# Performance work log

Measured on AMD Instinct MI355X. Metric: run time of the kernel, lower is better.

The kernel has to match this reference:

```python
import jax, jax.numpy as jnp
import numpy as np

EPS = 1e-5

def gelu(x):
    return jax.nn.gelu(x, approximate=False)  # torch nn.GELU default = exact erf

def bn(x, g, b, m, v):
    # eval-mode BatchNorm1d with running stats; broadcasts over batch axis
    return (x - m) * jax.lax.rsqrt(v + EPS) * g + b

def ln(x, g, b):
    mu = jnp.mean(x, axis=-1, keepdims=True)
    var = jnp.var(x, axis=-1, keepdims=True)
    return (x - mu) * jax.lax.rsqrt(var + EPS) * g + b

def setup_inputs() -> dict:
    B, D, H, E, C = 4096, 512, 1024, 16, 20  # combined dim D = wifi(256)+rfid(256)
    key = jax.random.key(0)
    ks = iter(jax.random.split(key, 40))
    n = lambda shape, s=0.02: jax.random.normal(next(ks), shape, dtype=jnp.float32) * s
    u = lambda shape: jax.random.uniform(next(ks), shape, dtype=jnp.float32, minval=0.5, maxval=1.5)
    inp = {
        'wifi_feat': jax.random.normal(next(ks), (B, 256), dtype=jnp.float32),
        'rfid_feat': jax.random.normal(next(ks), (B, 256), dtype=jnp.float32),
        # gate: Linear(512,1024) -> LayerNorm -> GELU -> Linear(1024,16) -> Softmax
        'gate_w1': n((D, 1024)), 'gate_b1': n((1024,)),
        'gate_ln_g': 1.0 + n((1024,)), 'gate_ln_b': n((1024,)),
        'gate_w2': n((1024, E)), 'gate_b2': n((E,)),
        # experts stacked on leading E axis
        'exp_w1': n((E, D, H)), 'exp_b1': n((E, H)),
        'exp_bn1_g': 1.0 + n((E, H)), 'exp_bn1_b': n((E, H)), 'exp_bn1_m': n((E, H), 0.1), 'exp_bn1_v': u((E, H)),
        'exp_w2': n((E, H, H)), 'exp_b2': n((E, H)),
        'exp_bn2_g': 1.0 + n((E, H)), 'exp_bn2_b': n((E, H)), 'exp_bn2_m': n((E, H), 0.1), 'exp_bn2_v': u((E, H)),
        # final head: Linear(1024,512) -> BN -> GELU -> Linear(512,20)
        'fin_w1': n((H, 512)), 'fin_b1': n((512,)),
        'fin_bn_g': 1.0 + n((512,)), 'fin_bn_b': n((512,)), 'fin_bn_m': n((512,), 0.1), 'fin_bn_v': u((512,)),
        'fin_w2': n((512, C)), 'fin_b2': n((C,)),
    }
    return inp

def reference(wifi_feat, rfid_feat,
              gate_w1, gate_b1, gate_ln_g, gate_ln_b, gate_w2, gate_b2,
              exp_w1, exp_b1, exp_bn1_g, exp_bn1_b, exp_bn1_m, exp_bn1_v,
              exp_w2, exp_b2, exp_bn2_g, exp_bn2_b, exp_bn2_m, exp_bn2_v,
              fin_w1, fin_b1, fin_bn_g, fin_bn_b, fin_bn_m, fin_bn_v,
              fin_w2, fin_b2):
    TOPK = 4
    combined = jnp.concatenate([wifi_feat, rfid_feat], axis=1)  # [B, 512]
    # gate
    g = gelu(ln(combined @ gate_w1 + gate_b1, gate_ln_g, gate_ln_b))
    gate = jax.nn.softmax(g @ gate_w2 + gate_b2, axis=1)  # [B, E]
    topk_gate, topk_idx = jax.lax.top_k(gate, TOPK)  # sorted, matches torch.topk
    topk_gate = jax.nn.softmax(topk_gate, axis=1)  # [B, K]
    # dense all-expert stack (faithful to original torch.stack over experts)
    h = jnp.einsum('bi,eih->ebh', combined, exp_w1) + exp_b1[:, None, :]  # [E,B,H]
    h = gelu(bn(h, exp_bn1_g[:, None, :], exp_bn1_b[:, None, :], exp_bn1_m[:, None, :], exp_bn1_v[:, None, :]))
    h = jnp.einsum('ebh,eho->ebo', h, exp_w2) + exp_b2[:, None, :]
    h = gelu(bn(h, exp_bn2_g[:, None, :], exp_bn2_b[:, None, :], exp_bn2_m[:, None, :], exp_bn2_v[:, None, :]))
    expert_outputs = jnp.transpose(h, (1, 0, 2))  # [B, E, H]
    selected = jnp.take_along_axis(expert_outputs, topk_idx[:, :, None], axis=1)  # [B,K,H]
    fused = jnp.einsum('bkd,bk->bd', selected, topk_gate)  # [B, H]
    # final head
    o = gelu(bn(fused @ fin_w1 + fin_b1, fin_bn_g, fin_bn_b, fin_bn_m, fin_bn_v))
    return o @ fin_w2 + fin_b2  # [B, num_classes]
```

## Files before the change

kernel.cpp:

```cpp
#include <hip/hip_runtime.h>


#define EPSN 1e-5f

typedef __attribute__((ext_vector_type(8))) short v8s;
typedef __attribute__((ext_vector_type(4))) float v4f;

typedef const unsigned int __attribute__((address_space(1)))* gas_u32;
typedef unsigned int __attribute__((address_space(3)))* las_u32;

__device__ __forceinline__ void glds16(const void* g, const void* l) {
    __builtin_amdgcn_global_load_lds((gas_u32)(uintptr_t)g, (las_u32)(uintptr_t)l, 16, 0, 0);
}

__device__ __forceinline__ float gelu_f(float x) {
    return 0.5f * x * (1.0f + erff(x * 0.70710678118654752440f));
}
__device__ __forceinline__ unsigned short f2bf(float x) {
    unsigned int u = __float_as_uint(x);
    u += 0x7fffu + ((u >> 16) & 1u);
    return (unsigned short)(u >> 16);
}
__device__ __forceinline__ float bf2f(unsigned short u) {
    return __uint_as_float(((unsigned int)u) << 16);
}

__global__ __launch_bounds__(256) void concat_kernel(const float4* __restrict__ wifi,
                                                     const float4* __restrict__ rfid,
                                                     float4* __restrict__ comb,
                                                     ushort4* __restrict__ cbf,
                                                     ushort4* __restrict__ cbf3) {
    int gid = blockIdx.x * 256 + threadIdx.x;
    int b = gid >> 7, c = gid & 127;
    float4 v = (c < 64) ? wifi[b * 64 + c] : rfid[b * 64 + (c - 64)];
    comb[gid] = v;
    ushort4 hi, lo;
    hi.x = f2bf(v.x); hi.y = f2bf(v.y); hi.z = f2bf(v.z); hi.w = f2bf(v.w);
    lo.x = f2bf(v.x - bf2f(hi.x));
    lo.y = f2bf(v.y - bf2f(hi.y));
    lo.z = f2bf(v.z - bf2f(hi.z));
    lo.w = f2bf(v.w - bf2f(hi.w));
    cbf[gid] = hi;
    const long r3 = (long)b * 384 + c;
    cbf3[r3]       = hi;
    cbf3[r3 + 128] = lo;
    cbf3[r3 + 256] = hi;
}

__global__ __launch_bounds__(256) void transpose_f2b(const float* __restrict__ in,
                                                     unsigned short* __restrict__ out,
                                                     int K, int N) {
    __shared__ float t[64][65];
    int e = blockIdx.z;
    int n0 = blockIdx.x << 6, k0 = blockIdx.y << 6;
    const float* ie = in + (long)e * K * N;
    unsigned short* oe = out + (long)e * N * K;
    int tid = threadIdx.x;
    int rr = tid >> 4, cc = (tid & 15) << 2;
#pragma unroll
    for (int p = 0; p < 4; ++p) {
        int k = (p << 4) + rr;
        float4 v = *(const float4*)(ie + (long)(k0 + k) * N + n0 + cc);
        t[k][cc + 0] = v.x; t[k][cc + 1] = v.y; t[k][cc + 2] = v.z; t[k][cc + 3] = v.w;
    }
    __syncthreads();
    int n = tid >> 2, kq = (tid & 3) << 4;
    unsigned short u[16];
#pragma unroll
    for (int j = 0; j < 16; ++j) u[j] = f2bf(t[kq + j][n]);
    uint4* dst = (uint4*)(oe + (long)(n0 + n) * K + k0 + kq);
    dst[0] = ((const uint4*)u)[0];
    dst[1] = ((const uint4*)u)[1];
}

__global__ __launch_bounds__(256) void transpose_f2b_hilo(const float* __restrict__ in,
                                                          unsigned short* __restrict__ out,
                                                          int K, int N) {
    __shared__ float t[64][65];
    int n0 = blockIdx.x << 6, k0 = blockIdx.y << 6;
    int tid = threadIdx.x;
    int rr = tid >> 4, cc = (tid & 15) << 2;
#pragma unroll
    for (int p = 0; p < 4; ++p) {
        int k = (p << 4) + rr;
        float4 v = *(const float4*)(in + (long)(k0 + k) * N + n0 + cc);
        t[k][cc + 0] = v.x; t[k][cc + 1] = v.y; t[k][cc + 2] = v.z; t[k][cc + 3] = v.w;
    }
    __syncthreads();
    int n = tid >> 2, kq = (tid & 3) << 4;
    unsigned short uh[16], ul[16];
#pragma unroll
    for (int j = 0; j < 16; ++j) {
        float x = t[kq + j][n];
        unsigned short h = f2bf(x);
        uh[j] = h;
        ul[j] = f2bf(x - bf2f(h));
    }
    unsigned short* dh = out + (long)(n0 + n) * (3 * K) + k0 + kq;
    ((uint4*)dh)[0]           = ((const uint4*)uh)[0];
    ((uint4*)dh)[1]           = ((const uint4*)uh)[1];
    ((uint4*)(dh + K))[0]     = ((const uint4*)uh)[0];
    ((uint4*)(dh + K))[1]     = ((const uint4*)uh)[1];
    ((uint4*)(dh + 2 * K))[0] = ((const uint4*)ul)[0];
    ((uint4*)(dh + 2 * K))[1] = ((const uint4*)ul)[1];
}

__global__ __launch_bounds__(256) void transpose_w2g(const float* __restrict__ in,
                                                     float* __restrict__ out) {
    int gid = blockIdx.x * 256 + threadIdx.x;
    int c = gid >> 4, e = gid & 15;
    out[e * 1024 + c] = in[gid];
}

__global__ __launch_bounds__(256) void ln_topk_wave(
    const float* __restrict__ g,
    const float* __restrict__ lng, const float* __restrict__ lnb,
    const float* __restrict__ w2t, const float* __restrict__ b2,
    float* __restrict__ wout, unsigned int* __restrict__ topk)
{
    const int tid = threadIdx.x;
    const int lane = tid & 63;
    const int b = (blockIdx.x << 2) + (tid >> 6);
    const float* row = g + (long)b * 1024;
    const int c0 = lane << 2;

    float4 xv[4];
    float s = 0.f, q = 0.f;
#pragma unroll
    for (int p = 0; p < 4; ++p) {
        float4 v = *(const float4*)(row + (p << 8) + c0);
        xv[p] = v;
        s += v.x + v.y + v.z + v.w;
        q += v.x * v.x + v.y * v.y + v.z * v.z + v.w * v.w;
    }
#pragma unroll
    for (int mk = 32; mk >= 1; mk >>= 1) {
        s += __shfl_xor(s, mk);
        q += __shfl_xor(q, mk);
    }
    const float mu = s * (1.0f / 1024.0f);
    const float var = q * (1.0f / 1024.0f) - mu * mu;
    const float rstd = rsqrtf(var + EPSN);

#pragma unroll
    for (int p = 0; p < 4; ++p) {
        float4 gv = *(const float4*)(lng + (p << 8) + c0);
        float4 bv = *(const float4*)(lnb + (p << 8) + c0);
        xv[p].x = gelu_f((xv[p].x - mu) * rstd * gv.x + bv.x);
        xv[p].y = gelu_f((xv[p].y - mu) * rstd * gv.y + bv.y);
        xv[p].z = gelu_f((xv[p].z - mu) * rstd * gv.z + bv.z);
        xv[p].w = gelu_f((xv[p].w - mu) * rstd * gv.w + bv.w);
    }

    float a[16];
#pragma unroll
    for (int i = 0; i < 16; ++i) a[i] = 0.f;
#pragma unroll
    for (int p = 0; p < 4; ++p) {
        const float4 x4 = xv[p];
        const float* wp = w2t + (p << 8) + c0;
#pragma unroll
        for (int e = 0; e < 16; ++e) {
            const float4 w = *(const float4*)(wp + (e << 10));
            a[e] = fmaf(x4.x, w.x, a[e]);
            a[e] = fmaf(x4.y, w.y, a[e]);
            a[e] = fmaf(x4.z, w.z, a[e]);
            a[e] = fmaf(x4.w, w.w, a[e]);
        }
    }
#pragma unroll
    for (int mk = 32; mk >= 1; mk >>= 1) {
#pragma unroll
        for (int i = 0; i < 16; ++i) a[i] += __shfl_xor(a[i], mk);
    }
#pragma unroll
    for (int i = 0; i < 16; ++i) a[i] += b2[i];

    float m = a[0];
#pragma unroll
    for (int i = 1; i < 16; ++i) m = fmaxf(m, a[i]);
    float Z = 0.f;
#pragma unroll
    for (int i = 0; i < 16; ++i) { a[i] = expf(a[i] - m); Z += a[i]; }
    const float iZ = 1.0f / Z;
#pragma unroll
    for (int i = 0; i < 16; ++i) a[i] *= iZ;

    float tv0, tv1, tv2, tv3;
    int ti0, ti1, ti2, ti3;
#define PICK(TV, TI)                                                         \
    {   float bv = a[0]; int bi = 0;                                         \
        _Pragma("unroll")                                                    \
        for (int i = 1; i < 16; ++i) {                                       \
            bool t = a[i] > bv; bv = t ? a[i] : bv; bi = t ? i : bi;         \
        }                                                                    \
        TV = bv; TI = bi;                                                    \
        _Pragma("unroll")                                                    \
        for (int i = 0; i < 16; ++i) a[i] = (i == bi) ? -1.f : a[i];         \
    }
    PICK(tv0, ti0)
    PICK(tv1, ti1)
    PICK(tv2, ti2)
    PICK(tv3, ti3)
#undef PICK

    const float q1 = expf(tv1 - tv0);
    const float q2 = expf(tv2 - tv0);
    const float q3 = expf(tv3 - tv0);
    const float iZ2 = 1.0f / (1.0f + q1 + q2 + q3);
    if (lane < 4) {
        float wk = (lane == 0) ? 1.f : (lane == 1) ? q1 : (lane == 2) ? q2 : q3;
        wout[(b << 2) + lane] = wk * iZ2;
    }
    if (lane == 0)
        topk[b] = (unsigned)ti0 | ((unsigned)ti1 << 8) |
                  ((unsigned)ti2 << 16) | ((unsigned)ti3 << 24);
}

__global__ __launch_bounds__(256) void compact_kernel(const unsigned int* __restrict__ topk,
                                                      int* __restrict__ rows_,
                                                      int* __restrict__ counts) {
    const int e = blockIdx.x;
    const int tid = threadIdx.x;
    const int wid = tid >> 6, lane = tid & 63;
    __shared__ int wcnt[4];
    __shared__ int wbase[4];
    __shared__ int running;
    if (tid == 0) running = 0;
    __syncthreads();
    for (int c = 0; c < 16; ++c) {
        const int r = (c << 8) + tid;
        const unsigned int w = topk[r];
        int slot = -1;
        if (((w >> 0)  & 255u) == (unsigned)e) slot = (r << 2) | 0;
        if (((w >> 8)  & 255u) == (unsigned)e) slot = (r << 2) | 1;
        if (((w >> 16) & 255u) == (unsigned)e) slot = (r << 2) | 2;
        if (((w >> 24) & 255u) == (unsigned)e) slot = (r << 2) | 3;
        const unsigned long long m = __ballot(slot >= 0);
        if (lane == 0) wcnt[wid] = __popcll(m);
        __syncthreads();
        if (tid == 0) {
            int base = running;
#pragma unroll
            for (int i = 0; i < 4; ++i) { wbase[i] = base; base += wcnt[i]; }
            running = base;
        }
        __syncthreads();
        if (slot >= 0) {
            const int pref = __popcll(m & ((1ull << lane) - 1ull));
            rows_[(e << 12) + wbase[wid] + pref] = slot;
        }
        __syncthreads();
    }
    if (tid == 0) counts[e] = running;
}

#define WLG 1024
__global__ __launch_bounds__(256) void build_wl_kernel(const int* __restrict__ counts,
                                                       int* __restrict__ wl) {
    int t = threadIdx.x;
    for (int i = t; i < 8 * WLG; i += 256) wl[i] = -1;
    __syncthreads();
    if (t < 8) {
        int* wg = wl + (t << 10);
        int idx = 0;
#pragma unroll
        for (int half = 0; half < 2; ++half) {
            int e = t + (half << 3);
            int nc = (counts[e] + 63) >> 6;
            for (int mc = 0; mc < nc; ++mc)
                for (int x = 0; x < 8; ++x)
                    wg[idx++] = (e << 16) | (mc << 4) | x;
        }
    }
}

template<int ASHIFT, bool GATHER, bool OUTBF, bool WL, bool PLAIN = false>
__global__ __launch_bounds__(256) void mfma_gemm(
    const unsigned short* __restrict__ A, int K,
    const unsigned short* __restrict__ Wt, long wstride,
    const float* __restrict__ bias,
    const float* __restrict__ bng, const float* __restrict__ bnb,
    const float* __restrict__ bnm, const float* __restrict__ bnv,
    int pstride,
    void* __restrict__ outv, int ldo,
    const int* __restrict__ rows_, const int* __restrict__ counts,
    const int* __restrict__ wl, int M)
{
    constexpr int TM = 64;
    int e, m0, n0;
    if constexpr (WL) {
        int w = wl[((blockIdx.x & 7) << 10) | (blockIdx.x >> 3)];
        if (w < 0) return;
        e = w >> 16;
        m0 = ((w >> 4) & 0xfff) << 6;
        n0 = (w & 15) << 7;
    } else {
        e = blockIdx.y;
        m0 = blockIdx.x * TM;
        n0 = blockIdx.z << 7;
    }
    const int cnt = GATHER ? counts[e] : M;

    constexpr int AB_USH = 64 * 64 + 128 * 64;
    constexpr int OL_STRIDE = 136;
    constexpr int OL_USH = OUTBF ? TM * OL_STRIDE : 0;
    constexpr int SM_USH = (OL_USH > AB_USH) ? OL_USH : AB_USH;
    __shared__ __align__(16) unsigned short smem[SM_USH];
    unsigned short* Als = smem;
    unsigned short* Bls = smem + 64 * 64;
    __shared__ int rid[TM];
    __shared__ int ain[TM];

    const int tid = threadIdx.x;
    if (tid < TM) {
        int i = m0 + tid;
        int pk, ai;
        if (GATHER) {
            if (i < cnt) { pk = rows_[(e << 12) + i]; ai = pk >> ASHIFT; }
            else { pk = -1; ai = 0; }
        } else { pk = i; ai = i; }
        rid[tid] = pk;
        ain[tid] = ai;
    }
    __syncthreads();

    const int wave = tid >> 6, lane = tid & 63;
    const int wm = (wave >> 1) << 5, wn = (wave & 1) << 6;
    const int lrow = lane & 15, kch = lane >> 4;
    const int wb = wave << 9;

    const int srow = tid >> 3, spos = tid & 7;
    const int skc8 = (spos ^ (srow & 7)) << 3;

    const unsigned short* apa = A + (long)ain[srow] * K + skc8;
    const unsigned short* apb = A + (long)ain[32 + srow] * K + skc8;
    const unsigned short* Wte = Wt + (long)e * wstride;
    const unsigned short* bp0 = Wte + (long)(n0 + srow) * K + skc8;
    const unsigned short* bp1 = Wte + (long)(n0 + 32 + srow) * K + skc8;
    const unsigned short* bp2 = Wte + (long)(n0 + 64 + srow) * K + skc8;
    const unsigned short* bp3 = Wte + (long)(n0 + 96 + srow) * K + skc8;

    v4f acc[2][4] = {};

    const int nk = K >> 6;
    for (int it = 0; it < nk; ++it) {
        glds16(apa, Als + wb);
        glds16(apb, Als + 2048 + wb);
        glds16(bp0, Bls + wb);
        glds16(bp1, Bls + 2048 + wb);
        glds16(bp2, Bls + 4096 + wb);
        glds16(bp3, Bls + 6144 + wb);
        apa += 64; apb += 64; bp0 += 64; bp1 += 64; bp2 += 64; bp3 += 64;
        __syncthreads();

#pragma unroll
        for (int s = 0; s < 2; ++s) {
            const int kc = (s << 2) | kch;
            v8s av[2], bv[4];
#pragma unroll
            for (int f = 0; f < 2; ++f) {
                const int row = wm + (f << 4) + lrow;
                av[f] = *(const v8s*)(Als + row * 64 + ((kc ^ (row & 7)) << 3));
            }
#pragma unroll
            for (int f = 0; f < 4; ++f) {
                const int row = wn + (f << 4) + lrow;
                bv[f] = *(const v8s*)(Bls + row * 64 + ((kc ^ (row & 7)) << 3));
            }
#pragma unroll
            for (int fi = 0; fi < 2; ++fi)
#pragma unroll
                for (int fj = 0; fj < 4; ++fj)
                    acc[fi][fj] = __builtin_amdgcn_mfma_f32_16x16x32_bf16(
                        av[fi], bv[fj], acc[fi][fj], 0, 0, 0);
        }
        __syncthreads();
    }

    if constexpr (OUTBF) {
        unsigned short* Ols = smem;
#pragma unroll
        for (int fj = 0; fj < 4; ++fj) {
            const int c = wn + (fj << 4) + lrow;
            const int pc = e * pstride + n0 + c;
            const float bs = bias[pc];
            const float sc = bng[pc] * rsqrtf(bnv[pc] + EPSN);
            const float mn = bnm[pc], bb = bnb[pc];
#pragma unroll
            for (int fi = 0; fi < 2; ++fi) {
#pragma unroll
                for (int r = 0; r < 4; ++r) {
                    const int lr = wm + (fi << 4) + (kch << 2) + r;
                    float x = acc[fi][fj][r] + bs;
                    x = (x - mn) * sc + bb;
                    x = gelu_f(x);
                    Ols[lr * OL_STRIDE + c] = f2bf(x);
                }
            }
        }
        __syncthreads();
        const int rl = tid >> 4;
        const int c8 = (tid & 15) << 3;
#pragma unroll
        for (int p = 0; p < TM / 16; ++p) {
            const int row = (p << 4) + rl;
            const int orow = rid[row];
            if (orow >= 0) {
                uint4 v = *(const uint4*)(Ols + row * OL_STRIDE + c8);
                *(uint4*)((unsigned short*)outv + (long)orow * ldo + n0 + c8) = v;
            }
        }
    } else {
#pragma unroll
        for (int fj = 0; fj < 4; ++fj) {
            const int c = n0 + wn + (fj << 4) + lrow;
            const int pc = e * pstride + c;
            const float bs = bias[pc];
            float sc = 1.f, mn = 0.f, bb = 0.f;
            if constexpr (!PLAIN) {
                sc = bng[pc] * rsqrtf(bnv[pc] + EPSN);
                mn = bnm[pc]; bb = bnb[pc];
            }
#pragma unroll
            for (int fi = 0; fi < 2; ++fi) {
#pragma unroll
                for (int r = 0; r < 4; ++r) {
                    const int lr = wm + (fi << 4) + (kch << 2) + r;
                    const int orow = rid[lr];
                    if (orow < 0) continue;
                    float x = acc[fi][fj][r] + bs;
                    if constexpr (!PLAIN) {
                        x = (x - mn) * sc + bb;
                        x = gelu_f(x);
                    }
                    ((float*)outv)[(long)orow * ldo + c] = x;
                }
            }
        }
    }
}

__global__ __launch_bounds__(256) void combine_bf_kernel(const ushort4* __restrict__ h2b,
                                                         const float* __restrict__ w,
                                                         ushort4* __restrict__ fusedb) {
    int gid = blockIdx.x * 256 + threadIdx.x;
    int b = gid >> 8, c = gid & 255;
    float a0 = 0.f, a1 = 0.f, a2 = 0.f, a3 = 0.f;
#pragma unroll
    for (int k = 0; k < 4; ++k) {
        float wk = w[b * 4 + k];
        ushort4 v = h2b[(long)(b * 4 + k) * 256 + c];
        a0 += wk * bf2f(v.x); a1 += wk * bf2f(v.y);
        a2 += wk * bf2f(v.z); a3 += wk * bf2f(v.w);
    }
    ushort4 o;
    o.x = f2bf(a0); o.y = f2bf(a1); o.z = f2bf(a2); o.w = f2bf(a3);
    fusedb[gid] = o;
}

__global__ __launch_bounds__(256) void fin2_kernel(const float* __restrict__ o,
                                                   const float* __restrict__ w2,
                                                   const float* __restrict__ b2,
                                                   float* __restrict__ out) {
    __shared__ float ws[512 * 20];
    int tid = threadIdx.x;
    for (int i = tid; i < 512 * 20; i += 256) ws[i] = w2[i];
    __syncthreads();
    int r = blockIdx.x * 64 + (tid >> 2);
    int c0 = (tid & 3) * 5;
    float acc[5];
#pragma unroll
    for (int j = 0; j < 5; ++j) acc[j] = b2[c0 + j];
    const float* orow = o + (long)r * 512;
    for (int i = 0; i < 512; ++i) {
        float v = orow[i];
#pragma unroll
        for (int j = 0; j < 5; ++j) acc[j] += v * ws[i * 20 + c0 + j];
    }
#pragma unroll
    for (int j = 0; j < 5; ++j) out[r * 20 + c0 + j] = acc[j];
}

extern "C" void kernel_launch(void* const* d_in, const int* in_sizes, int n_in,
                              void* d_out, int out_size, void* d_ws, size_t ws_size,
                              hipStream_t stream) {
    const float* wifi    = (const float*)d_in[0];
    const float* rfid    = (const float*)d_in[1];
    const float* gate_w1 = (const float*)d_in[2];
    const float* gate_b1 = (const float*)d_in[3];
    const float* gln_g   = (const float*)d_in[4];
    const float* gln_b   = (const float*)d_in[5];
    const float* gate_w2 = (const float*)d_in[6];
    const float* gate_b2 = (const float*)d_in[7];
    const float* exp_w1  = (const float*)d_in[8];
    const float* exp_b1  = (const float*)d_in[9];
    const float* bn1g    = (const float*)d_in[10];
    const float* bn1b    = (const float*)d_in[11];
    const float* bn1m    = (const float*)d_in[12];
    const float* bn1v    = (const float*)d_in[13];
    const float* exp_w2  = (const float*)d_in[14];
    const float* exp_b2  = (const float*)d_in[15];
    const float* bn2g    = (const float*)d_in[16];
    const float* bn2b    = (const float*)d_in[17];
    const float* bn2m    = (const float*)d_in[18];
    const float* bn2v    = (const float*)d_in[19];
    const float* fin_w1  = (const float*)d_in[20];
    const float* fin_b1  = (const float*)d_in[21];
    const float* fbng    = (const float*)d_in[22];
    const float* fbnb    = (const float*)d_in[23];
    const float* fbnm    = (const float*)d_in[24];
    const float* fbnv    = (const float*)d_in[25];
    const float* fin_w2  = (const float*)d_in[26];
    const float* fin_b2  = (const float*)d_in[27];
    float* out = (float*)d_out;

    const size_t MBy = 1u << 20;
    char* W = (char*)d_ws;
    float*          combined = (float*)         (W + 0);
    unsigned short* cbf      = (unsigned short*)(W + 8 * MBy);
    unsigned short* w1t      = (unsigned short*)(W + 12 * MBy);
    unsigned short* fusedb   = (unsigned short*)(W + 12 * MBy);
    float*          obuf     = (float*)         (W + 20 * MBy);
    unsigned short* w2t      = (unsigned short*)(W + 29 * MBy);
    float*          wq       = (float*)         (W + 61 * MBy);
    int*            rows     = (int*)           (W + 61 * MBy + (1 << 16));
    int*            counts   = (int*)           (W + 61 * MBy + (1 << 16) + (1 << 18));
    int*            wl       = (int*)           (W + 61 * MBy + (1 << 16) + (1 << 18) + 256);
    unsigned int*   topk     = (unsigned int*)  (W + 61 * MBy + (6 << 16));
    float*          w2tg     = (float*)         (W + 62 * MBy);
    unsigned short* fw1t     = (unsigned short*)(W + 63 * MBy);
    unsigned short* h1bf     = (unsigned short*)(W + 65 * MBy);
    unsigned short* cbf3     = (unsigned short*)(W + 65 * MBy);
    unsigned short* w1t3     = (unsigned short*)(W + 77 * MBy);
    float*          gbuf     = (float*)         (W + 99 * MBy);
    unsigned short* h2b      = (unsigned short*)(W + 99 * MBy);

    concat_kernel<<<2048, 256, 0, stream>>>((const float4*)wifi, (const float4*)rfid,
                                            (float4*)combined, (ushort4*)cbf,
                                            (ushort4*)cbf3);

    transpose_f2b<<<dim3(16, 8, 16), 256, 0, stream>>>(exp_w1, w1t, 512, 1024);
    transpose_f2b<<<dim3(16, 16, 16), 256, 0, stream>>>(exp_w2, w2t, 1024, 1024);
    transpose_f2b<<<dim3(8, 16, 1), 256, 0, stream>>>(fin_w1, fw1t, 1024, 512);
    transpose_f2b_hilo<<<dim3(16, 8, 1), 256, 0, stream>>>(gate_w1, w1t3, 512, 1024);
    transpose_w2g<<<64, 256, 0, stream>>>(gate_w2, w2tg);

    mfma_gemm<0, false, false, false, true><<<dim3(64, 1, 8), 256, 0, stream>>>(
        cbf3, 1536, w1t3, 0, gate_b1,
        nullptr, nullptr, nullptr, nullptr, 0,
        gbuf, 1024, nullptr, nullptr, nullptr, 4096);

    ln_topk_wave<<<1024, 256, 0, stream>>>(gbuf, gln_g, gln_b, w2tg, gate_b2,
                                           wq, topk);
    compact_kernel<<<16, 256, 0, stream>>>(topk, rows, counts);
    build_wl_kernel<<<1, 256, 0, stream>>>(counts, wl);

    mfma_gemm<2, true, true, true><<<dim3(8 * WLG, 1, 1), 256, 0, stream>>>(
        cbf, 512, w1t, (long)512 * 1024, exp_b1,
        bn1g, bn1b, bn1m, bn1v, 1024,
        h1bf, 1024, rows, counts, wl, 4096);

    mfma_gemm<0, true, true, true><<<dim3(8 * WLG, 1, 1), 256, 0, stream>>>(
        h1bf, 1024, w2t, (long)1024 * 1024, exp_b2,
        bn2g, bn2b, bn2m, bn2v, 1024,
        h2b, 1024, rows, counts, wl, 4096);

    combine_bf_kernel<<<4096, 256, 0, stream>>>((const ushort4*)h2b, wq, (ushort4*)fusedb);

    mfma_gemm<0, false, false, false><<<dim3(64, 1, 4), 256, 0, stream>>>(
        fusedb, 1024, fw1t, 0, fin_b1,
        fbng, fbnb, fbnm, fbnv, 0,
        obuf, 512, nullptr, nullptr, nullptr, 4096);

    fin2_kernel<<<64, 256, 0, stream>>>(obuf, fin_w2, fin_b2, out);
}
```

Measured before the change: 445.4 us.

## Double-buffer LDS tiles in expert GEMM to overlap global loads with MFMA

```diff
diff --git a/kernel.cpp b/kernel.cpp
--- a/kernel.cpp
+++ b/kernel.cpp
@@ -302,13 +302,12 @@
     }
     const int cnt = GATHER ? counts[e] : M;
 
-    constexpr int AB_USH = 64 * 64 + 128 * 64;
+    constexpr int BUF = 64 * 64 + 128 * 64;
+    constexpr int AB_USH = 2 * BUF;
     constexpr int OL_STRIDE = 136;
     constexpr int OL_USH = OUTBF ? TM * OL_STRIDE : 0;
     constexpr int SM_USH = (OL_USH > AB_USH) ? OL_USH : AB_USH;
     __shared__ __align__(16) unsigned short smem[SM_USH];
-    unsigned short* Als = smem;
-    unsigned short* Bls = smem + 64 * 64;
     __shared__ int rid[TM];
     __shared__ int ain[TM];
 
@@ -341,19 +340,33 @@
     const unsigned short* bp2 = Wte + (long)(n0 + 64 + srow) * K + skc8;
     const unsigned short* bp3 = Wte + (long)(n0 + 96 + srow) * K + skc8;
 
+#define STAGE(d)                                                         \
+    {   unsigned short* Ad = smem + (d) * BUF;                           \
+        unsigned short* Bd = Ad + 64 * 64;                               \
+        glds16(apa, Ad + wb);                                            \
+        glds16(apb, Ad + 2048 + wb);                                     \
+        glds16(bp0, Bd + wb);                                            \
+        glds16(bp1, Bd + 2048 + wb);                                     \
+        glds16(bp2, Bd + 4096 + wb);                                     \
+        glds16(bp3, Bd + 6144 + wb);                                     \
+        apa += 64; apb += 64; bp0 += 64; bp1 += 64; bp2 += 64; bp3 += 64; }
+
     v4f acc[2][4] = {};
 
     const int nk = K >> 6;
+    STAGE(0)
     for (int it = 0; it < nk; ++it) {
-        glds16(apa, Als + wb);
-        glds16(apb, Als + 2048 + wb);
-        glds16(bp0, Bls + wb);
-        glds16(bp1, Bls + 2048 + wb);
-        glds16(bp2, Bls + 4096 + wb);
-        glds16(bp3, Bls + 6144 + wb);
-        apa += 64; apb += 64; bp0 += 64; bp1 += 64; bp2 += 64; bp3 += 64;
-        __syncthreads();
-
+        const int cur = it & 1;
+        if (it + 1 < nk) {
+            STAGE(cur ^ 1)
+            asm volatile("s_waitcnt vmcnt(6)" ::: "memory");
+        } else {
+            asm volatile("s_waitcnt vmcnt(0)" ::: "memory");
+        }
+        asm volatile("s_barrier" ::: "memory");
+
+        const unsigned short* Als = smem + cur * BUF;
+        const unsigned short* Bls = Als + 64 * 64;
 #pragma unroll
         for (int s = 0; s < 2; ++s) {
             const int kc = (s << 2) | kch;
@@ -375,8 +388,9 @@
                     acc[fi][fj] = __builtin_amdgcn_mfma_f32_16x16x32_bf16(
                         av[fi], bv[fj], acc[fi][fj], 0, 0, 0);
         }
-        __syncthreads();
-    }
+        asm volatile("s_barrier" ::: "memory");
+    }
+#undef STAGE
 
     if constexpr (OUTBF) {
         unsigned short* Ols = smem;
```

After: 438.2 us. No clear change (-1.6%).

## Enlarge GEMM M-tile to 128 rows with 4x4 MFMA fragments per wave

Applied to the files above, without the earlier changes.

```diff
diff --git a/kernel.cpp b/kernel.cpp
--- a/kernel.cpp
+++ b/kernel.cpp
@@ -267,7 +267,7 @@
 #pragma unroll
         for (int half = 0; half < 2; ++half) {
             int e = t + (half << 3);
-            int nc = (counts[e] + 63) >> 6;
+            int nc = (counts[e] + 127) >> 7;
             for (int mc = 0; mc < nc; ++mc)
                 for (int x = 0; x < 8; ++x)
                     wg[idx++] = (e << 16) | (mc << 4) | x;
@@ -287,13 +287,13 @@
     const int* __restrict__ rows_, const int* __restrict__ counts,
     const int* __restrict__ wl, int M)
 {
-    constexpr int TM = 64;
+    constexpr int TM = 128;
     int e, m0, n0;
     if constexpr (WL) {
         int w = wl[((blockIdx.x & 7) << 10) | (blockIdx.x >> 3)];
         if (w < 0) return;
         e = w >> 16;
-        m0 = ((w >> 4) & 0xfff) << 6;
+        m0 = ((w >> 4) & 0xfff) << 7;
         n0 = (w & 15) << 7;
     } else {
         e = blockIdx.y;
@@ -302,13 +302,10 @@
     }
     const int cnt = GATHER ? counts[e] : M;
 
-    constexpr int AB_USH = 64 * 64 + 128 * 64;
+    constexpr int A_USH = 128 * 64;
+    constexpr int AB_USH = 2 * A_USH;
     constexpr int OL_STRIDE = 136;
-    constexpr int OL_USH = OUTBF ? TM * OL_STRIDE : 0;
-    constexpr int SM_USH = (OL_USH > AB_USH) ? OL_USH : AB_USH;
-    __shared__ __align__(16) unsigned short smem[SM_USH];
-    unsigned short* Als = smem;
-    unsigned short* Bls = smem + 64 * 64;
+    __shared__ __align__(16) unsigned short smem[AB_USH];
     __shared__ int rid[TM];
     __shared__ int ain[TM];
 
@@ -326,50 +323,55 @@
     __syncthreads();
 
     const int wave = tid >> 6, lane = tid & 63;
-    const int wm = (wave >> 1) << 5, wn = (wave & 1) << 6;
+    const int wm = (wave >> 1) << 6, wn = (wave & 1) << 6;
     const int lrow = lane & 15, kch = lane >> 4;
     const int wb = wave << 9;
 
     const int srow = tid >> 3, spos = tid & 7;
     const int skc8 = (spos ^ (srow & 7)) << 3;
 
-    const unsigned short* apa = A + (long)ain[srow] * K + skc8;
-    const unsigned short* apb = A + (long)ain[32 + srow] * K + skc8;
+    const unsigned short* ap0 = A + (long)ain[srow] * K + skc8;
+    const unsigned short* ap1 = A + (long)ain[32 + srow] * K + skc8;
+    const unsigned short* ap2 = A + (long)ain[64 + srow] * K + skc8;
+    const unsigned short* ap3 = A + (long)ain[96 + srow] * K + skc8;
     const unsigned short* Wte = Wt + (long)e * wstride;
-    const unsigned short* bp0 = Wte + (long)(n0 + srow) * K + skc8;
-    const unsigned short* bp1 = Wte + (long)(n0 + 32 + srow) * K + skc8;
-    const unsigned short* bp2 = Wte + (long)(n0 + 64 + srow) * K + skc8;
-    const unsigned short* bp3 = Wte + (long)(n0 + 96 + srow) * K + skc8;
-
-    v4f acc[2][4] = {};
+    const unsigned short* bq0 = Wte + (long)(n0 + srow) * K + skc8;
+    const unsigned short* bq1 = Wte + (long)(n0 + 32 + srow) * K + skc8;
+    const unsigned short* bq2 = Wte + (long)(n0 + 64 + srow) * K + skc8;
+    const unsigned short* bq3 = Wte + (long)(n0 + 96 + srow) * K + skc8;
+
+    unsigned short* Als = smem;
+    unsigned short* Bls = smem + A_USH;
+
+    v4f acc[4][4] = {};
 
     const int nk = K >> 6;
     for (int it = 0; it < nk; ++it) {
-        glds16(apa, Als + wb);
-        glds16(apb, Als + 2048 + wb);
-        glds16(bp0, Bls + wb);
-        glds16(bp1, Bls + 2048 + wb);
-        glds16(bp2, Bls + 4096 + wb);
-        glds16(bp3, Bls + 6144 + wb);
-        apa += 64; apb += 64; bp0 += 64; bp1 += 64; bp2 += 64; bp3 += 64;
+        glds16(ap0, Als + wb);
+        glds16(ap1, Als + 2048 + wb);
+        glds16(ap2, Als + 4096 + wb);
+        glds16(ap3, Als + 6144 + wb);
+        glds16(bq0, Bls + wb);
+        glds16(bq1, Bls + 2048 + wb);
+        glds16(bq2, Bls + 4096 + wb);
+        glds16(bq3, Bls + 6144 + wb);
+        ap0 += 64; ap1 += 64; ap2 += 64; ap3 += 64;
+        bq0 += 64; bq1 += 64; bq2 += 64; bq3 += 64;
         __syncthreads();
 
 #pragma unroll
         for (int s = 0; s < 2; ++s) {
             const int kc = (s << 2) | kch;
-            v8s av[2], bv[4];
-#pragma unroll
-            for (int f = 0; f < 2; ++f) {
-                const int row = wm + (f << 4) + lrow;
-                av[f] = *(const v8s*)(Als + row * 64 + ((kc ^ (row & 7)) << 3));
-            }
-#pragma unroll
-            for (int f = 0; f < 4; ++f) {
-                const int row = wn + (f << 4) + lrow;
-                bv[f] = *(const v8s*)(Bls + row * 64 + ((kc ^ (row & 7)) << 3));
-            }
-#pragma unroll
-            for (int fi = 0; fi < 2; ++fi)
+            const int sw = (kc ^ (lrow & 7)) << 3;
+            v8s av[4], bv[4];
+#pragma unroll
+            for (int f = 0; f < 4; ++f)
+                av[f] = *(const v8s*)(Als + (wm + (f << 4) + lrow) * 64 + sw);
+#pragma unroll
+            for (int f = 0; f < 4; ++f)
+                bv[f] = *(const v8s*)(Bls + (wn + (f << 4) + lrow) * 64 + sw);
+#pragma unroll
+            for (int fi = 0; fi < 4; ++fi)
 #pragma unroll
                 for (int fj = 0; fj < 4; ++fj)
                     acc[fi][fj] = __builtin_amdgcn_mfma_f32_16x16x32_bf16(
@@ -381,35 +383,41 @@
     if constexpr (OUTBF) {
         unsigned short* Ols = smem;
 #pragma unroll
-        for (int fj = 0; fj < 4; ++fj) {
-            const int c = wn + (fj << 4) + lrow;
-            const int pc = e * pstride + n0 + c;
-            const float bs = bias[pc];
-            const float sc = bng[pc] * rsqrtf(bnv[pc] + EPSN);
-            const float mn = bnm[pc], bb = bnb[pc];
-#pragma unroll
-            for (int fi = 0; fi < 2; ++fi) {
-#pragma unroll
-                for (int r = 0; r < 4; ++r) {
-                    const int lr = wm + (fi << 4) + (kch << 2) + r;
-                    float x = acc[fi][fj][r] + bs;
-                    x = (x - mn) * sc + bb;
-                    x = gelu_f(x);
-                    Ols[lr * OL_STRIDE + c] = f2bf(x);
+        for (int h = 0; h < 2; ++h) {
+            if ((wave >> 1) == h) {
+#pragma unroll
+                for (int fj = 0; fj < 4; ++fj) {
+                    const int c = wn + (fj << 4) + lrow;
+                    const int pc = e * pstride + n0 + c;
+                    const float bs = bias[pc];
+                    const float sc = bng[pc] * rsqrtf(bnv[pc] + EPSN);
+                    const float mn = bnm[pc], bb = bnb[pc];
+#pragma unroll
+                    for (int fi = 0; fi < 4; ++fi) {
+#pragma unroll
+                        for (int r = 0; r < 4; ++r) {
+                            const int lrl = (fi << 4) + (kch << 2) + r;
+                            float x = acc[fi][fj][r] + bs;
+                            x = (x - mn) * sc + bb;
+                            x = gelu_f(x);
+                            Ols[lrl * OL_STRIDE + c] = f2bf(x);
+                        }
+                    }
                 }
             }
-        }
-        __syncthreads();
-        const int rl = tid >> 4;
-        const int c8 = (tid & 15) << 3;
-#pragma unroll
-        for (int p = 0; p < TM / 16; ++p) {
-            const int row = (p << 4) + rl;
-            const int orow = rid[row];
-            if (orow >= 0) {
-                uint4 v = *(const uint4*)(Ols + row * OL_STRIDE + c8);
-                *(uint4*)((unsigned short*)outv + (long)orow * ldo + n0 + c8) = v;
+            __syncthreads();
+            const int rl = tid >> 4;
+            const int c8 = (tid & 15) << 3;
+#pragma unroll
+            for (int p = 0; p < 4; ++p) {
+                const int row = (p << 4) + rl;
+                const int orow = rid[(h << 6) + row];
+                if (orow >= 0) {
+                    uint4 v = *(const uint4*)(Ols + row * OL_STRIDE + c8);
+                    *(uint4*)((unsigned short*)outv + (long)orow * ldo + n0 + c8) = v;
+                }
             }
+            __syncthreads();
         }
     } else {
 #pragma unroll
@@ -423,7 +431,7 @@
                 mn = bnm[pc]; bb = bnb[pc];
             }
 #pragma unroll
-            for (int fi = 0; fi < 2; ++fi) {
+            for (int fi = 0; fi < 4; ++fi) {
 #pragma unroll
                 for (int r = 0; r < 4; ++r) {
                     const int lr = wm + (fi << 4) + (kch << 2) + r;
@@ -546,7 +554,7 @@
     transpose_f2b_hilo<<<dim3(16, 8, 1), 256, 0, stream>>>(gate_w1, w1t3, 512, 1024);
     transpose_w2g<<<64, 256, 0, stream>>>(gate_w2, w2tg);
 
-    mfma_gemm<0, false, false, false, true><<<dim3(64, 1, 8), 256, 0, stream>>>(
+    mfma_gemm<0, false, false, false, true><<<dim3(32, 1, 8), 256, 0, stream>>>(
         cbf3, 1536, w1t3, 0, gate_b1,
         nullptr, nullptr, nullptr, nullptr, 0,
         gbuf, 1024, nullptr, nullptr, nullptr, 4096);
@@ -556,19 +564,19 @@
     compact_kernel<<<16, 256, 0, stream>>>(topk, rows, counts);
     build_wl_kernel<<<1, 256, 0, stream>>>(counts, wl);
 
-    mfma_gemm<2, true, true, true><<<dim3(8 * WLG, 1, 1), 256, 0, stream>>>(
+    mfma_gemm<2, true, true, true><<<dim3(4096, 1, 1), 256, 0, stream>>>(
         cbf, 512, w1t, (long)512 * 1024, exp_b1,
         bn1g, bn1b, bn1m, bn1v, 1024,
         h1bf, 1024, rows, counts, wl, 4096);
 
-    mfma_gemm<0, true, true, true><<<dim3(8 * WLG, 1, 1), 256, 0, stream>>>(
+    mfma_gemm<0, true, true, true><<<dim3(4096, 1, 1), 256, 0, stream>>>(
         h1bf, 1024, w2t, (long)1024 * 1024, exp_b2,
         bn2g, bn2b, bn2m, bn2v, 1024,
         h2b, 1024, rows, counts, wl, 4096);
 
     combine_bf_kernel<<<4096, 256, 0, stream>>>((const ushort4*)h2b, wq, (ushort4*)fusedb);
 
-    mfma_gemm<0, false, false, false><<<dim3(64, 1, 4), 256, 0, stream>>>(
+    mfma_gemm<0, false, false, false><<<dim3(32, 1, 4), 256, 0, stream>>>(
         fusedb, 1024, fw1t, 0, fin_b1,
         fbng, fbnb, fbnm, fbnv, 0,
         obuf, 512, nullptr, nullptr, nullptr, 4096);
```

After: 740.3 us. 66.2% more time.

## Compact expert work list, shrink GEMM grids, and streamline top-k row compaction

Applied to the files above, without the earlier changes.

```diff
diff --git a/kernel.cpp b/kernel.cpp
--- a/kernel.cpp
+++ b/kernel.cpp
@@ -27,13 +27,11 @@
 
 __global__ __launch_bounds__(256) void concat_kernel(const float4* __restrict__ wifi,
                                                      const float4* __restrict__ rfid,
-                                                     float4* __restrict__ comb,
                                                      ushort4* __restrict__ cbf,
                                                      ushort4* __restrict__ cbf3) {
     int gid = blockIdx.x * 256 + threadIdx.x;
     int b = gid >> 7, c = gid & 127;
     float4 v = (c < 64) ? wifi[b * 64 + c] : rfid[b * 64 + (c - 64)];
-    comb[gid] = v;
     ushort4 hi, lo;
     hi.x = f2bf(v.x); hi.y = f2bf(v.y); hi.z = f2bf(v.z); hi.w = f2bf(v.w);
     lo.x = f2bf(v.x - bf2f(hi.x));
@@ -223,55 +221,58 @@
     const int e = blockIdx.x;
     const int tid = threadIdx.x;
     const int wid = tid >> 6, lane = tid & 63;
-    __shared__ int wcnt[4];
-    __shared__ int wbase[4];
-    __shared__ int running;
-    if (tid == 0) running = 0;
+    __shared__ int wtot[4];
+
+    int cw = 0;
+#pragma unroll
+    for (int it = 0; it < 16; ++it) {
+        const int r = (wid << 10) + (it << 6) + lane;
+        const unsigned int w = topk[r];
+        bool hit = (((w) & 255u) == (unsigned)e) | (((w >> 8) & 255u) == (unsigned)e) |
+                   (((w >> 16) & 255u) == (unsigned)e) | (((w >> 24) & 255u) == (unsigned)e);
+        cw += __popcll(__ballot(hit));
+    }
+    if (lane == 0) wtot[wid] = cw;
     __syncthreads();
-    for (int c = 0; c < 16; ++c) {
-        const int r = (c << 8) + tid;
+    int base = 0;
+#pragma unroll
+    for (int j = 0; j < 4; ++j) base += (j < wid) ? wtot[j] : 0;
+    if (tid == 0) counts[e] = wtot[0] + wtot[1] + wtot[2] + wtot[3];
+
+    int off = base;
+#pragma unroll
+    for (int it = 0; it < 16; ++it) {
+        const int r = (wid << 10) + (it << 6) + lane;
         const unsigned int w = topk[r];
         int slot = -1;
-        if (((w >> 0)  & 255u) == (unsigned)e) slot = (r << 2) | 0;
-        if (((w >> 8)  & 255u) == (unsigned)e) slot = (r << 2) | 1;
+        if (((w) & 255u) == (unsigned)e)       slot = (r << 2) | 0;
+        if (((w >> 8) & 255u) == (unsigned)e)  slot = (r << 2) | 1;
         if (((w >> 16) & 255u) == (unsigned)e) slot = (r << 2) | 2;
         if (((w >> 24) & 255u) == (unsigned)e) slot = (r << 2) | 3;
         const unsigned long long m = __ballot(slot >= 0);
-        if (lane == 0) wcnt[wid] = __popcll(m);
-        __syncthreads();
-        if (tid == 0) {
-            int base = running;
-#pragma unroll
-            for (int i = 0; i < 4; ++i) { wbase[i] = base; base += wcnt[i]; }
-            running = base;
-        }
-        __syncthreads();
         if (slot >= 0) {
             const int pref = __popcll(m & ((1ull << lane) - 1ull));
-            rows_[(e << 12) + wbase[wid] + pref] = slot;
+            rows_[(e << 12) + off + pref] = slot;
         }
-        __syncthreads();
-    }
-    if (tid == 0) counts[e] = running;
-}
-
-#define WLG 1024
+        off += __popcll(m);
+    }
+}
+
+#define WL_MAX 2176
 __global__ __launch_bounds__(256) void build_wl_kernel(const int* __restrict__ counts,
                                                        int* __restrict__ wl) {
     int t = threadIdx.x;
-    for (int i = t; i < 8 * WLG; i += 256) wl[i] = -1;
+    for (int i = t; i < WL_MAX; i += 256) wl[i] = -1;
     __syncthreads();
-    if (t < 8) {
-        int* wg = wl + (t << 10);
-        int idx = 0;
-#pragma unroll
-        for (int half = 0; half < 2; ++half) {
-            int e = t + (half << 3);
-            int nc = (counts[e] + 63) >> 6;
-            for (int mc = 0; mc < nc; ++mc)
-                for (int x = 0; x < 8; ++x)
-                    wg[idx++] = (e << 16) | (mc << 4) | x;
-        }
+    int off[17];
+    off[0] = 0;
+#pragma unroll
+    for (int e = 0; e < 16; ++e) off[e + 1] = off[e] + (((counts[e] + 63) >> 6) << 3);
+    const int e = t >> 4, s = t & 15;
+    const int ne = ((counts[e] + 63) >> 6) << 3;
+    for (int i = s; i < ne; i += 16) {
+        int mc = i >> 3, x = i & 7;
+        wl[off[e] + i] = (e << 16) | (mc << 4) | x;
     }
 }
 
@@ -290,7 +291,7 @@
     constexpr int TM = 64;
     int e, m0, n0;
     if constexpr (WL) {
-        int w = wl[((blockIdx.x & 7) << 10) | (blockIdx.x >> 3)];
+        int w = wl[blockIdx.x];
         if (w < 0) return;
         e = w >> 16;
         m0 = ((w >> 4) & 0xfff) << 6;
@@ -517,7 +518,6 @@
 
     const size_t MBy = 1u << 20;
     char* W = (char*)d_ws;
-    float*          combined = (float*)         (W + 0);
     unsigned short* cbf      = (unsigned short*)(W + 8 * MBy);
     unsigned short* w1t      = (unsigned short*)(W + 12 * MBy);
     unsigned short* fusedb   = (unsigned short*)(W + 12 * MBy);
@@ -537,8 +537,7 @@
     unsigned short* h2b      = (unsigned short*)(W + 99 * MBy);
 
     concat_kernel<<<2048, 256, 0, stream>>>((const float4*)wifi, (const float4*)rfid,
-                                            (float4*)combined, (ushort4*)cbf,
-                                            (ushort4*)cbf3);
+                                            (ushort4*)cbf, (ushort4*)cbf3);
 
     transpose_f2b<<<dim3(16, 8, 16), 256, 0, stream>>>(exp_w1, w1t, 512, 1024);
     transpose_f2b<<<dim3(16, 16, 16), 256, 0, stream>>>(exp_w2, w2t, 1024, 1024);
@@ -556,12 +555,12 @@
     compact_kernel<<<16, 256, 0, stream>>>(topk, rows, counts);
     build_wl_kernel<<<1, 256, 0, stream>>>(counts, wl);
 
-    mfma_gemm<2, true, true, true><<<dim3(8 * WLG, 1, 1), 256, 0, stream>>>(
+    mfma_gemm<2, true, true, true><<<dim3(WL_MAX, 1, 1), 256, 0, stream>>>(
         cbf, 512, w1t, (long)512 * 1024, exp_b1,
         bn1g, bn1b, bn1m, bn1v, 1024,
         h1bf, 1024, rows, counts, wl, 4096);
 
-    mfma_gemm<0, true, true, true><<<dim3(8 * WLG, 1, 1), 256, 0, stream>>>(
+    mfma_gemm<0, true, true, true><<<dim3(WL_MAX, 1, 1), 256, 0, stream>>>(
         h1bf, 1024, w2t, (long)1024 * 1024, exp_b2,
         bn2g, bn2b, bn2m, bn2v, 1024,
         h2b, 1024, rows, counts, wl, 4096);
```

Measured after the change: 424.5 us. -4.7%, faster.
